# Kernel optimization log

Hardware: AMD Instinct MI355X
Metric: run time of the kernel (lower is better)

Reference implementation:

```python
import jax, jax.numpy as jnp
import numpy as np

NUM_CLASSES = 80
IOU_THR = 0.5
SCORE_THR = 0.25
MAX_BBOXES = 100
NEG = -1e9  # sentinel for suppressed scores


def setup_inputs() -> dict:
    key = jax.random.key(0)
    ks = jax.random.split(key, 9)
    B = 8
    def head(i, g):
        return (jax.random.uniform(ks[3*i], (B, g, g, 3, 4), dtype=jnp.float32),
                jax.random.uniform(ks[3*i+1], (B, g, g, 3, 1), dtype=jnp.float32),
                jax.random.normal(ks[3*i+2], (B, g, g, 3, NUM_CLASSES), dtype=jnp.float32))
    b20, p20, c20 = head(0, 20)
    b40, p40, c40 = head(1, 40)
    b80, p80, c80 = head(2, 80)
    return {"bbox20": b20, "p20": p20, "c20": c20,
            "bbox40": b40, "p40": p40, "c40": c40,
            "bbox80": b80, "p80": p80, "c80": c80}


def _iou_one_vs_all(box, boxes):
    # box: (4,) [y1,x1,y2,x2]; boxes: (N,4)
    y1, x1, y2, x2 = box[0], box[1], box[2], box[3]
    Y1, X1, Y2, X2 = boxes[:, 0], boxes[:, 1], boxes[:, 2], boxes[:, 3]
    ih = jnp.maximum(jnp.minimum(y2, Y2) - jnp.maximum(y1, Y1), 0.0)
    iw = jnp.maximum(jnp.minimum(x2, X2) - jnp.maximum(x1, X1), 0.0)
    inter = ih * iw
    union = (y2 - y1) * (x2 - x1) + (Y2 - Y1) * (X2 - X1) - inter
    return jnp.where(union > 0, inter / union, 0.0)


def _nms_single(boxes, scores):
    # boxes (N,4), scores (N,) -> greedy class-agnostic NMS, up to MAX_BBOXES
    sc0 = jnp.where(scores > SCORE_THR, scores, NEG)

    def body(sc, _):
        idx = jnp.argmax(sc)
        s = sc[idx]
        valid = s > NEG * 0.5
        box = boxes[idx]
        iou = _iou_one_vs_all(box, boxes)
        sc = jnp.where(iou > IOU_THR, NEG, sc)
        sc = sc.at[idx].set(NEG)
        ob = jnp.where(valid, jnp.clip(box, 0.0, 1.0), 0.0)  # clip_boxes=True default
        os = jnp.where(valid, s, 0.0)
        return sc, (ob, os, valid)

    _, (b, s, v) = jax.lax.scan(body, sc0, None, length=MAX_BBOXES)
    return b, s, jnp.sum(v.astype(jnp.int32))


def _forward(bbox20, p20, c20, bbox40, p40, c40, bbox80, p80, c80):
    B = bbox20.shape[0]
    bbox = jnp.concatenate([x.reshape(B, -1, 4) for x in (bbox20, bbox40, bbox80)], axis=1)
    p = jnp.concatenate([x.reshape(B, -1) for x in (p20, p40, p80)], axis=1)
    c = jnp.concatenate([x.reshape(B, -1, NUM_CLASSES) for x in (c20, c40, c80)], axis=1)
    cls = jnp.argmax(c, axis=-1).astype(jnp.float32)  # (B,N)
    score = p * cls  # quirky score = objectness * class index (faithful to source)
    b, s, valid = jax.vmap(_nms_single)(bbox, score)
    # classes output: scores had a single class dim in the TF op -> class index 0
    pred = jnp.concatenate([b, s[..., None], jnp.zeros_like(s)[..., None]], axis=-1)
    return pred, valid


def reference(bbox20, p20, c20, bbox40, p40, c40, bbox80, p80, c80):
    return _forward(bbox20, p20, c20, bbox40, p40, c40, bbox80, p80, c80)
```

## Files before the change

kernel.cpp:

```cpp
#include <hip/hip_runtime.h>

#define NUM_CLASSES 80
#define BATCH 8
#define N20 1200
#define N40 4800
#define N80 19200
#define NANCH 25200
#define NEGV  -1000000000.0f
#define SCORE_THR 0.25f
#define CAP 2048
#define RMAX 192
#define PKCAP 512
#define NHBIN 1024
#define THR_LIST 64.0f
#define NBLK 99
#define NSLOT 396
#define SLOTCAP 32

typedef unsigned long long ull;

__global__ __launch_bounds__(256, 3) void score_kernel(
        const float* __restrict__ p20, const float* __restrict__ c20,
        const float* __restrict__ p40, const float* __restrict__ c40,
        const float* __restrict__ p80, const float* __restrict__ c80,
        float* __restrict__ scores, unsigned* __restrict__ gcnt,
        ull* __restrict__ gkeys) {
    const int t = threadIdx.x;
    const int b = blockIdx.y;
    const int an = blockIdx.x * 256 + t;
    const bool valid_an = (an < NANCH);
    const int n = valid_an ? an : (NANCH - 1);

    const float *cp, *pp;
    if (n < N20) {
        cp = c20 + ((size_t)b * N20 + n) * NUM_CLASSES;
        pp = p20 + (size_t)b * N20 + n;
    } else if (n < N20 + N40) {
        int a = n - N20;
        cp = c40 + ((size_t)b * N40 + a) * NUM_CLASSES;
        pp = p40 + (size_t)b * N40 + a;
    } else {
        int a = n - N20 - N40;
        cp = c80 + ((size_t)b * N80 + a) * NUM_CLASSES;
        pp = p80 + (size_t)b * N80 + a;
    }

    const float4* c4 = (const float4*)cp;
    float p = *pp;
    float4 v[20];
#pragma unroll
    for (int k = 0; k < 20; k++) v[k] = c4[k];
    __builtin_amdgcn_sched_barrier(0);

    float best = -INFINITY;
    int bi = 0;
#pragma unroll
    for (int k = 0; k < 20; k++) {
        int basei = k * 4;
        if (v[k].x > best) { best = v[k].x; bi = basei; }
        if (v[k].y > best) { best = v[k].y; bi = basei + 1; }
        if (v[k].z > best) { best = v[k].z; bi = basei + 2; }
        if (v[k].w > best) { best = v[k].w; bi = basei + 3; }
    }

    float s = __fmul_rn(p, (float)bi);
    float sval = (s > SCORE_THR) ? s : NEGV;
    if (valid_an) scores[(size_t)b * NANCH + an] = sval;

    const bool cand = valid_an && (sval >= THR_LIST);
    const ull mask = __ballot(cand);
    const int lane = t & 63;
    const int slot = blockIdx.x * 4 + (t >> 6);
    if (cand) {
        const int pos = __popcll(mask & ((1ull << lane) - 1ull));
        if (pos < SLOTCAP) {
            const ull key = ((ull)__float_as_uint(sval) << 32) |
                            (ull)(0xFFFFFFFFu - (unsigned)an);
            gkeys[(((size_t)b * NSLOT + slot) << 5) + pos] = key;
        }
    }
    if (lane == 0) gcnt[b * NSLOT + slot] = (unsigned)__popcll(mask);
}

__device__ __forceinline__ bool iou_gt(const float4 A, float areaA, const float4 Bx, float areaB) {
    float ih = fmaxf(__fsub_rn(fminf(A.z, Bx.z), fmaxf(A.x, Bx.x)), 0.0f);
    float iw = fmaxf(__fsub_rn(fminf(A.w, Bx.w), fmaxf(A.y, Bx.y)), 0.0f);
    float inter = __fmul_rn(ih, iw);
    float uni = __fsub_rn(__fadd_rn(areaA, areaB), inter);
    if (!(uni > 0.0f)) return false;
    return __fdiv_rn(inter, uni) > 0.5f;
}

__device__ __forceinline__ bool iou_gt_fast(const float4 A, float areaA, const float4 Bx, float areaB) {
    float ih = fmaxf(__fsub_rn(fminf(A.z, Bx.z), fmaxf(A.x, Bx.x)), 0.0f);
    float iw = fmaxf(__fsub_rn(fminf(A.w, Bx.w), fmaxf(A.y, Bx.y)), 0.0f);
    float inter = __fmul_rn(ih, iw);
    float uni = __fsub_rn(__fadd_rn(areaA, areaB), inter);
    if (!(uni > 0.0f)) return false;
    if (__fmul_rn(2.0f, inter) < __fmul_rn(uni, 0.99999988f)) return false;
    return __fdiv_rn(inter, uni) > 0.5f;
}

__device__ __forceinline__ float4 load_box(int b, int n,
        const float* b20, const float* b40, const float* b80) {
    if (n < N20)       return ((const float4*)b20)[(size_t)b * N20 + n];
    if (n < N20 + N40) return ((const float4*)b40)[(size_t)b * N40 + (n - N20)];
    return ((const float4*)b80)[(size_t)b * N80 + (n - N20 - N40)];
}

__device__ __forceinline__ float box_area(const float4 B) {
    return __fmul_rn(__fsub_rn(B.z, B.x), __fsub_rn(B.w, B.y));
}

__device__ __forceinline__ int key_idx(ull k) {
    return (int)(0xFFFFFFFFu - (unsigned)(k & 0xFFFFFFFFull));
}

__global__ __launch_bounds__(1024) void nms_kernel(
        float* __restrict__ scores, const unsigned* __restrict__ gcnt,
        const ull* __restrict__ gkeys,
        const float* __restrict__ b20, const float* __restrict__ b40,
        const float* __restrict__ b80, float* __restrict__ out) {
    __shared__ ull skeys[CAP];
    __shared__ ull pk[PKCAP];
    __shared__ unsigned hist[NHBIN];
    __shared__ int prt[PKCAP][5];
    __shared__ ull srt_key[RMAX];
    __shared__ float4 bboxC[4][RMAX + 1];
    __shared__ ull M[RMAX][3];
    __shared__ unsigned scnt[NSLOT];
    __shared__ unsigned soff[NSLOT];
    __shared__ int sh_V, sh_T, sh_m, sh_ovf;
    __shared__ unsigned sh_pcnt;

    const int t = threadIdx.x;
    const int lane = t & 63;
    const int b = blockIdx.x;

    hist[t] = 0u;
    if (t == 0) { sh_V = 0; sh_ovf = 0; sh_pcnt = 0u; }
    __syncthreads();

    if (t < NSLOT) {
        unsigned c = gcnt[b * NSLOT + t];
        scnt[t] = c;
        if (c > (unsigned)SLOTCAP) sh_ovf = 1;
    }
    __syncthreads();

    if (t < 64) {
        unsigned c[7];
        unsigned s = 0;
#pragma unroll
        for (int k = 0; k < 7; k++) {
            int idx = t * 7 + k;
            c[k] = (idx < NSLOT) ? scnt[idx] : 0u;
            s += c[k];
        }
        unsigned incl = s;
#pragma unroll
        for (int d = 1; d < 64; d <<= 1) {
            unsigned vv = __shfl_up(incl, d);
            if (t >= d) incl += vv;
        }
        unsigned base = incl - s;
#pragma unroll
        for (int k = 0; k < 7; k++) {
            int idx = t * 7 + k;
            if (idx < NSLOT) soff[idx] = base;
            base += c[k];
        }
        if (t == 63) sh_m = (int)incl;
    }
    __syncthreads();

    const int m = sh_m;
    const bool use_list = (m <= CAP) && (sh_ovf == 0);
    const int nR = use_list ? min(m, RMAX) : 0;
    const unsigned need = (unsigned)nR;

    if (use_list) {
        for (int c = t; c < m; c += 1024) {
            int lo = 0, hi = NSLOT - 1;
            while (lo < hi) {
                int mid = (lo + hi + 1) >> 1;
                if (soff[mid] <= (unsigned)c) lo = mid; else hi = mid - 1;
            }
            ull k = gkeys[(((size_t)b * NSLOT + lo) << 5) + (c - soff[lo])];
            skeys[c] = k;
            unsigned sb = (unsigned)(k >> 32);
            atomicAdd(&hist[min((int)((sb - 0x42800000u) >> 13), NHBIN - 1)], 1u);
        }
    }
    __syncthreads();

    if (use_list) {
        if (t < 64) {
            unsigned h[16], sfx[16];
            const int basei = t * 16;
#pragma unroll
            for (int k = 0; k < 16; k++) h[k] = hist[basei + k];
            unsigned run = 0;
#pragma unroll
            for (int k = 15; k >= 0; k--) { run += h[k]; sfx[k] = run; }
            unsigned s = run;
#pragma unroll
            for (int d = 1; d < 64; d <<= 1) {
                unsigned vv = __shfl_down(s, d);
                if (t + d < 64) s += vv;
            }
            const unsigned above = s - run;
            int bestb = -1;
#pragma unroll
            for (int k = 0; k < 16; k++)
                if (sfx[k] + above >= need) bestb = basei + k;
#pragma unroll
            for (int d = 32; d > 0; d >>= 1) {
                int o = __shfl_down(bestb, d);
                if (t + d < 64) bestb = max(bestb, o);
            }
            if (t == 0) sh_T = max(bestb, 0);
        }
        __syncthreads();
        const int T = sh_T;

#pragma unroll
        for (int h = 0; h < 2; h++) {
            const int c = t + h * 1024;
            bool part = false;
            ull k = 0ull;
            if (c < m) {
                k = skeys[c];
                int bin = min((int)(((unsigned)(k >> 32) - 0x42800000u) >> 13), NHBIN - 1);
                part = (bin >= T);
            }
            ull mask = __ballot(part);
            if (mask != 0ull) {
                int leader = (int)(__ffsll(mask) - 1);
                unsigned basep = 0;
                if (lane == leader) basep = atomicAdd(&sh_pcnt, (unsigned)__popcll(mask));
                basep = __shfl(basep, leader);
                if (part) {
                    unsigned pos = basep + (unsigned)__popcll(mask & ((1ull << lane) - 1));
                    if (pos < (unsigned)PKCAP) pk[pos] = k;
                }
            }
        }
        __syncthreads();
        const int pm = (int)sh_pcnt;

        if (pm <= PKCAP) {
            ull kmy = 0ull;
            float4 bmy = make_float4(0.f, 0.f, 0.f, 0.f);
            if (t < pm) {
                kmy = pk[t];
                bmy = load_box(b, key_idx(kmy), b20, b40, b80);
            }
            const int q = t >> 8, u = t & 255;
            const ull kA = (u < pm) ? pk[u] : 0ull;
            const ull kB = (u + 256 < pm) ? pk[u + 256] : 0ull;
            const int Q = (pm + 3) >> 2;
            const int j0 = q * Q, j1 = min(pm, j0 + Q);
            int rA = 0, rB = 0;
#pragma unroll 8
            for (int j = j0; j < j1; j++) {
                ull kj = pk[j];
                rA += (kj > kA) ? 1 : 0;
                rB += (kj > kB) ? 1 : 0;
            }
            prt[u][q] = rA;
            prt[u + 256][q] = rB;
            __syncthreads();
            if (t < pm) {
                int r = prt[t][0] + prt[t][1] + prt[t][2] + prt[t][3];
                if (r < RMAX) {
                    srt_key[r] = kmy;
#pragma unroll
                    for (int c = 0; c < 4; c++) bboxC[c][r] = bmy;
                }
            }
            __syncthreads();
        } else {
            ull kA = (t < m) ? skeys[t] : 0ull;
            ull kB = (t + 1024 < m) ? skeys[t + 1024] : 0ull;
            int rA = 0, rB = 0;
            for (int j = 0; j < m; j++) {
                ull kj = skeys[j];
                rA += (kj > kA) ? 1 : 0;
                rB += (kj > kB) ? 1 : 0;
            }
            if (t < m && rA < RMAX) srt_key[rA] = kA;
            if (t + 1024 < m && rB < RMAX) srt_key[rB] = kB;
            __syncthreads();
            if (t < nR) {
                float4 B = load_box(b, key_idx(srt_key[t]), b20, b40, b80);
#pragma unroll
                for (int c = 0; c < 4; c++) bboxC[c][t] = B;
            }
            __syncthreads();
        }

        {
            const int row = t >> 2, cw = t & 3;
            if (row < RMAX && cw < 3) {
                ull w = 0ull;
                if (row < nR && cw * 64 < row) {
                    const float4 B = bboxC[cw][row];
                    const float aB = box_area(B);
                    const int jmax = min(64, row - cw * 64);
                    const float4* src = &bboxC[cw][cw * 64];
                    for (int j = 0; j < jmax; j++) {
                        const float4 C = src[j];
                        w |= ((ull)iou_gt_fast(C, box_area(C), B, aB)) << j;
                    }
                }
                M[row][cw] = w;
            }
        }
        __syncthreads();

        int v = 0;
        if (t < 64) {
            ull A0 = 0, A1 = 0, A2 = 0;
            for (int rg = 0; rg < 3 && v < 100; rg++) {
                const int rr = rg * 64 + t;
                const bool valid = (rr < nR);
                ull w0 = 0, w1 = 0, w2 = 0;
                if (valid) { w0 = M[rr][0]; w1 = M[rr][1]; w2 = M[rr][2]; }
                const ull mw = (rg == 0) ? w0 : (rg == 1) ? w1 : w2;
                const bool supE = !valid ||
                    (((w0 & A0) | (w1 & A1) | (w2 & A2)) != 0ull);
                ull alive = __ballot(!supE);
                while (alive != 0ull && v < 100) {
                    int c = (int)(__ffsll(alive) - 1);
                    ull supc = __ballot((bool)((mw >> c) & 1ull));
                    alive &= ~(supc | (1ull << c));
                    if (rg == 0) A0 |= 1ull << c;
                    else if (rg == 1) A1 |= 1ull << c;
                    else A2 |= 1ull << c;
                    if (t == c) {
                        const float4 B = bboxC[0][rr];
                        float* rowp = out + ((size_t)b * 100 + v) * 6;
                        rowp[0] = fminf(fmaxf(B.x, 0.f), 1.f);
                        rowp[1] = fminf(fmaxf(B.y, 0.f), 1.f);
                        rowp[2] = fminf(fmaxf(B.z, 0.f), 1.f);
                        rowp[3] = fminf(fmaxf(B.w, 0.f), 1.f);
                        rowp[4] = __uint_as_float((unsigned)(srt_key[rr] >> 32));
                        rowp[5] = 0.f;
                    }
                    v++;
                }
            }
            if (t == 0) sh_V = v;
        }
        __syncthreads();
    }

    const bool need_fb = (!use_list) || (sh_V < 100);
    if (need_fb) {
        ull* red = skeys;
        float* scb = scores + (size_t)b * NANCH;
        int v2 = 0;
        for (int k = 0; k < 100; k++) {
            ull bestk = 0ull;
            for (int i = t; i < NANCH; i += 1024) {
                float sv = scb[i];
                unsigned u = __float_as_uint(sv);
                u ^= (u & 0x80000000u) ? 0xFFFFFFFFu : 0x80000000u;
                ull key = ((ull)u << 32) | (ull)(0xFFFFFFFFu - (unsigned)i);
                if (key > bestk) bestk = key;
            }
            red[t] = bestk;
            __syncthreads();
            for (int ss = 512; ss > 0; ss >>= 1) {
                if (t < ss && red[t + ss] > red[t]) red[t] = red[t + ss];
                __syncthreads();
            }
            ull bk = red[0];
            __syncthreads();
            unsigned u = (unsigned)(bk >> 32);
            u ^= (u & 0x80000000u) ? 0x80000000u : 0xFFFFFFFFu;
            float s = __uint_as_float(u);
            int idx = (int)(0xFFFFFFFFu - (unsigned)(bk & 0xFFFFFFFFull));
            if (!(s > NEGV * 0.5f)) break;
            float4 B = load_box(b, idx, b20, b40, b80);
            float aB = box_area(B);
            for (int i = t; i < NANCH; i += 1024) {
                float sv = scb[i];
                if (sv > NEGV * 0.5f) {
                    float4 C = load_box(b, i, b20, b40, b80);
                    if (iou_gt(B, aB, C, box_area(C))) scb[i] = NEGV;
                }
            }
            if (t == 0) {
                scb[idx] = NEGV;
                float* rowp = out + ((size_t)b * 100 + k) * 6;
                rowp[0] = fminf(fmaxf(B.x, 0.f), 1.f);
                rowp[1] = fminf(fmaxf(B.y, 0.f), 1.f);
                rowp[2] = fminf(fmaxf(B.z, 0.f), 1.f);
                rowp[3] = fminf(fmaxf(B.w, 0.f), 1.f);
                rowp[4] = s;
                rowp[5] = 0.f;
            }
            v2++;
            __syncthreads();
        }
        __syncthreads();
        if (t == 0) sh_V = v2;
        __syncthreads();
    }

    const int V = sh_V;
    for (int i = V * 6 + t; i < 600; i += 1024) out[(size_t)b * 600 + i] = 0.f;
    if (t == 0) out[4800 + b] = (float)V;
}

extern "C" void kernel_launch(void* const* d_in, const int* in_sizes, int n_in,
                              void* d_out, int out_size, void* d_ws, size_t ws_size,
                              hipStream_t stream) {
    const float* b20 = (const float*)d_in[0];
    const float* p20 = (const float*)d_in[1];
    const float* c20 = (const float*)d_in[2];
    const float* b40 = (const float*)d_in[3];
    const float* p40 = (const float*)d_in[4];
    const float* c40 = (const float*)d_in[5];
    const float* b80 = (const float*)d_in[6];
    const float* p80 = (const float*)d_in[7];
    const float* c80 = (const float*)d_in[8];

    float*    scores = (float*)d_ws;
    unsigned* gcnt   = (unsigned*)((char*)d_ws + 806400);
    ull*      gkeys  = (ull*)((char*)d_ws + 806400 + 12672);

    dim3 sgrid((NANCH + 255) / 256, BATCH);
    score_kernel<<<sgrid, 256, 0, stream>>>(
        p20, c20, p40, c40, p80, c80, scores, gcnt, gkeys);

    nms_kernel<<<BATCH, 1024, 0, stream>>>(
        scores, gcnt, gkeys, b20, b40, b80, (float*)d_out);
}
```

Measured before the change: 144.9 us.

## Split IoU mask into 32-bit words and resolve greedy NMS by parallel fixpoint

The IoU suppression matrix is now built as 32-bit half-words over 1152 work items, so the pairwise work spreads across all 1024 threads instead of about 576. The serial one-candidate-per-iteration greedy resolution is replaced by a wave-parallel fixpoint. Each round accepts every undecided box whose higher-ranked suppressors are all decided, and drops any box that overlaps an accepted one. Output slots are then computed with popcount prefixes. A guard bound marks failure and sends the block to the fallback path, which adds complexity and risks falling back more often.

```diff
diff --git a/kernel.cpp b/kernel.cpp
--- a/kernel.cpp
+++ b/kernel.cpp
@@ -127,7 +127,7 @@
     __shared__ int prt[PKCAP][5];
     __shared__ ull srt_key[RMAX];
     __shared__ float4 bboxC[4][RMAX + 1];
-    __shared__ ull M[RMAX][3];
+    __shared__ unsigned M32[RMAX][7];
     __shared__ unsigned scnt[NSLOT];
     __shared__ unsigned soff[NSLOT];
     __shared__ int sh_V, sh_T, sh_m, sh_ovf;
@@ -300,58 +300,80 @@
             __syncthreads();
         }
 
-        {
-            const int row = t >> 2, cw = t & 3;
-            if (row < RMAX && cw < 3) {
-                ull w = 0ull;
-                if (row < nR && cw * 64 < row) {
-                    const float4 B = bboxC[cw][row];
-                    const float aB = box_area(B);
-                    const int jmax = min(64, row - cw * 64);
-                    const float4* src = &bboxC[cw][cw * 64];
-                    for (int j = 0; j < jmax; j++) {
-                        const float4 C = src[j];
-                        w |= ((ull)iou_gt_fast(C, box_area(C), B, aB)) << j;
+        for (int e = t; e < RMAX * 6; e += 1024) {
+            const int row = e / 6, hw = e - row * 6;
+            unsigned wbits = 0u;
+            const int j0 = hw * 32;
+            if (row < nR && j0 < row) {
+                const int cw = hw >> 1;
+                const float4 B = bboxC[cw][row];
+                const float aB = box_area(B);
+                const int jmax = min(32, row - j0);
+                const float4* src = &bboxC[cw][j0];
+                for (int j = 0; j < jmax; j++) {
+                    const float4 C = src[j];
+                    wbits |= ((unsigned)iou_gt_fast(C, box_area(C), B, aB)) << j;
+                }
+            }
+            M32[row][hw] = wbits;
+        }
+        __syncthreads();
+
+        if (t < 64) {
+            ull Af0 = 0ull, Af1 = 0ull, Af2 = 0ull;
+            bool fail = false;
+#pragma unroll
+            for (int rg = 0; rg < 3; rg++) {
+                const int rr = rg * 64 + t;
+                const ull w0 = (ull)M32[rr][0] | ((ull)M32[rr][1] << 32);
+                const ull w1 = (ull)M32[rr][2] | ((ull)M32[rr][3] << 32);
+                const ull w2 = (ull)M32[rr][4] | ((ull)M32[rr][5] << 32);
+                const ull mw = (rg == 0) ? w0 : (rg == 1) ? w1 : w2;
+                ull P = 0ull;
+                if (rg >= 1) P |= (w0 & Af0);
+                if (rg >= 2) P |= (w1 & Af1);
+                const bool valid = (rr < nR);
+                bool acc = false;
+                bool und = valid && (P == 0ull);
+                ull Ag = 0ull;
+                ull Um = __ballot(und);
+                int guard = 64;
+                while (Um != 0ull && guard-- > 0) {
+                    if (und) {
+                        if ((mw & Ag) != 0ull) und = false;
+                        else if ((mw & Um) == 0ull) { acc = true; und = false; }
                     }
-                }
-                M[row][cw] = w;
-            }
-        }
-        __syncthreads();
-
-        int v = 0;
-        if (t < 64) {
-            ull A0 = 0, A1 = 0, A2 = 0;
-            for (int rg = 0; rg < 3 && v < 100; rg++) {
-                const int rr = rg * 64 + t;
-                const bool valid = (rr < nR);
-                ull w0 = 0, w1 = 0, w2 = 0;
-                if (valid) { w0 = M[rr][0]; w1 = M[rr][1]; w2 = M[rr][2]; }
-                const ull mw = (rg == 0) ? w0 : (rg == 1) ? w1 : w2;
-                const bool supE = !valid ||
-                    (((w0 & A0) | (w1 & A1) | (w2 & A2)) != 0ull);
-                ull alive = __ballot(!supE);
-                while (alive != 0ull && v < 100) {
-                    int c = (int)(__ffsll(alive) - 1);
-                    ull supc = __ballot((bool)((mw >> c) & 1ull));
-                    alive &= ~(supc | (1ull << c));
-                    if (rg == 0) A0 |= 1ull << c;
-                    else if (rg == 1) A1 |= 1ull << c;
-                    else A2 |= 1ull << c;
-                    if (t == c) {
-                        const float4 B = bboxC[0][rr];
-                        float* rowp = out + ((size_t)b * 100 + v) * 6;
-                        rowp[0] = fminf(fmaxf(B.x, 0.f), 1.f);
-                        rowp[1] = fminf(fmaxf(B.y, 0.f), 1.f);
-                        rowp[2] = fminf(fmaxf(B.z, 0.f), 1.f);
-                        rowp[3] = fminf(fmaxf(B.w, 0.f), 1.f);
-                        rowp[4] = __uint_as_float((unsigned)(srt_key[rr] >> 32));
-                        rowp[5] = 0.f;
+                    Ag = __ballot(acc);
+                    Um = __ballot(und);
+                }
+                if (Um != 0ull) fail = true;
+                if (rg == 0) Af0 = Ag; else if (rg == 1) Af1 = Ag; else Af2 = Ag;
+            }
+            const int c0 = __popcll(Af0), c1 = __popcll(Af1);
+            const int total = c0 + c1 + __popcll(Af2);
+            const ull low = (1ull << t) - 1ull;
+            if (!fail) {
+#pragma unroll
+                for (int rg = 0; rg < 3; rg++) {
+                    const ull Af = (rg == 0) ? Af0 : (rg == 1) ? Af1 : Af2;
+                    if ((Af >> t) & 1ull) {
+                        const int v = ((rg >= 1) ? c0 : 0) + ((rg >= 2) ? c1 : 0) +
+                                      __popcll(Af & low);
+                        if (v < 100) {
+                            const int rr = rg * 64 + t;
+                            const float4 B = bboxC[0][rr];
+                            float* rowp = out + ((size_t)b * 100 + v) * 6;
+                            rowp[0] = fminf(fmaxf(B.x, 0.f), 1.f);
+                            rowp[1] = fminf(fmaxf(B.y, 0.f), 1.f);
+                            rowp[2] = fminf(fmaxf(B.z, 0.f), 1.f);
+                            rowp[3] = fminf(fmaxf(B.w, 0.f), 1.f);
+                            rowp[4] = __uint_as_float((unsigned)(srt_key[rr] >> 32));
+                            rowp[5] = 0.f;
+                        }
                     }
-                    v++;
-                }
-            }
-            if (t == 0) sh_V = v;
+                }
+            }
+            if (t == 0) sh_V = fail ? 0 : ((total < 100) ? total : 100);
         }
         __syncthreads();
     }
```

Result: faster. 132.1 us (-8.8%).
